# Kernel tuning notes

Measured on AMD Instinct MI355X. Metric: run time of the kernel, lower is better.

## Reference

```python
import jax, jax.numpy as jnp
import numpy as np

SEQ_LEN, BATCH, INPUT_SIZE, HIDDEN_SIZE = 512, 64, 1024, 1024


def setup_inputs() -> dict:
    key = jax.random.key(0)
    k1, k2, k3 = jax.random.split(key, 3)
    inp = jax.random.normal(k1, (SEQ_LEN, BATCH, INPUT_SIZE), dtype=jnp.float32)
    weight_ih = jax.random.normal(k2, (4 * HIDDEN_SIZE, INPUT_SIZE), dtype=jnp.float32) * 0.01
    weight_hh = jax.random.normal(k3, (4 * HIDDEN_SIZE, HIDDEN_SIZE), dtype=jnp.float32) * 0.01
    bias_ih = jnp.zeros((4 * HIDDEN_SIZE,), dtype=jnp.float32)
    bias_hh = jnp.zeros((4 * HIDDEN_SIZE,), dtype=jnp.float32)
    h0 = jnp.zeros((BATCH, HIDDEN_SIZE), dtype=jnp.float32)
    c0 = jnp.zeros((BATCH, HIDDEN_SIZE), dtype=jnp.float32)
    return {"input": inp, "weight_ih": weight_ih, "weight_hh": weight_hh,
            "bias_ih": bias_ih, "bias_hh": bias_hh, "h0": h0, "c0": c0}


def _lstm(input, weight_ih, weight_hh, bias_ih, bias_hh, h0, c0):
    H = weight_hh.shape[1]
    # Precompute input projections for all timesteps in one big GEMM: [T,B,4H]
    x_proj = jnp.einsum('tbi,gi->tbg', input, weight_ih) + bias_ih + bias_hh

    def step(carry, xg_t):
        h_prev, c_prev = carry
        gates = xg_t + h_prev @ weight_hh.T  # [B, 4H]
        i_g = jax.nn.sigmoid(gates[:, 0*H:1*H])
        f_g = jax.nn.sigmoid(gates[:, 1*H:2*H])
        g_g = jnp.tanh(gates[:, 2*H:3*H])
        o_g = jax.nn.sigmoid(gates[:, 3*H:4*H])
        c_cur = f_g * c_prev + i_g * g_g
        h_cur = o_g * jnp.tanh(c_cur)
        return (h_cur, c_cur), h_cur

    (h_last, c_last), outputs = jax.lax.scan(step, (h0, c0), x_proj)
    return outputs, (h_last[None], c_last[None])


def reference(input, weight_ih, weight_hh, bias_ih, bias_hh, h0, c0):
    return _lstm(input, weight_ih, weight_hh, bias_ih, bias_hh, h0, c0)
```

## Files before the change

### kernel.cpp

```cpp
#include <hip/hip_runtime.h>
#include <stdint.h>

#define SEQ    512
#define NBATCH 64
#define HID    1024
#define GDIM   4096

typedef __attribute__((ext_vector_type(4))) float          f32x4;
typedef __attribute__((ext_vector_type(8))) short          s16x8;
typedef __attribute__((ext_vector_type(4))) unsigned short u16x4;
typedef __attribute__((ext_vector_type(4))) unsigned int   u32x4;

#define MFMA_BF16(a,b,c) __builtin_amdgcn_mfma_f32_16x16x32_bf16((a),(b),(c),0,0,0)

__device__ __forceinline__ unsigned short f2bf(float f){
  union { float f; unsigned u; } v; v.f = f;
  unsigned r = v.u + 0x7fffu + ((v.u >> 16) & 1u);
  return (unsigned short)(r >> 16);
}

__device__ __forceinline__ void gload_lds16(const void* g, void* l){
  __builtin_amdgcn_global_load_lds((const __attribute__((address_space(1))) void*)g,
                                   (__attribute__((address_space(3))) void*)l,
                                   16, 0, 0);
}

__global__ __launch_bounds__(256) void cvt_bf16(const float* __restrict__ s,
                                                unsigned short* __restrict__ d, int n4){
  int i = blockIdx.x*256 + threadIdx.x;
  if (i >= n4) return;
  f32x4 v = *(const f32x4*)(s + (size_t)i*4);
  u16x4 o;
  o[0]=f2bf(v[0]); o[1]=f2bf(v[1]); o[2]=f2bf(v[2]); o[3]=f2bf(v[3]);
  *(u16x4*)(d + (size_t)i*4) = o;
}

__global__ __launch_bounds__(256) void init_state(const float* __restrict__ h0,
                                                  const float* __restrict__ c0,
                                                  unsigned short* __restrict__ hring,
                                                  float* __restrict__ cstate){
  int i = blockIdx.x*256 + threadIdx.x;
  hring[i]  = f2bf(h0[i]);
  cstate[i] = c0[i];
}

__global__ __launch_bounds__(256,1) void gemm_xproj(
    const unsigned short* __restrict__ A,
    const unsigned short* __restrict__ Bw,
    const float* __restrict__ bih, const float* __restrict__ bhh,
    float* __restrict__ C, int M)
{
  __shared__ unsigned short Al[2][128*64];
  __shared__ unsigned short Bl[2][128*64];

  const int bm = blockIdx.x >> 5;
  const int bn = blockIdx.x & 31;
  const int tid = threadIdx.x;
  const int wv = tid >> 6, l = tid & 63;
  const int wm = wv >> 1, wn = wv & 1;
  const int c16 = l & 15, rq = l >> 4;

  const unsigned short* Ab = A  + (size_t)bm*128*1024;
  const unsigned short* Bb = Bw + (size_t)bn*128*1024;

  f32x4 acc[4][4];
#pragma unroll
  for (int i=0;i<4;++i)
#pragma unroll
    for (int j=0;j<4;++j) acc[i][j] = (f32x4){0.f,0.f,0.f,0.f};

  auto stage = [&](int buf, int kt){
    const int k0 = kt*64;
    const int rsub = wv*8 + (l>>3);
    const int col  = (l&7)*8;
#pragma unroll
    for (int is=0; is<4; ++is){
      const int row = is*32 + rsub;
      gload_lds16(Ab + (size_t)row*1024 + k0 + col, &Al[buf][row*64 + col]);
      gload_lds16(Bb + (size_t)row*1024 + k0 + col, &Bl[buf][row*64 + col]);
    }
  };

  stage(0, 0);
  asm volatile("s_waitcnt vmcnt(0)" ::: "memory");
  __syncthreads();

  for (int kt = 0; kt < 16; ++kt){
    const int cur = kt & 1;
    if (kt < 15) stage(cur^1, kt+1);
#pragma unroll
    for (int ks=0; ks<2; ++ks){
      s16x8 afr[4], bfr[4];
#pragma unroll
      for (int mi=0;mi<4;++mi)
        afr[mi] = *(const s16x8*)&Al[cur][(wm*64 + mi*16 + c16)*64 + ks*32 + rq*8];
#pragma unroll
      for (int ni=0;ni<4;++ni)
        bfr[ni] = *(const s16x8*)&Bl[cur][(wn*64 + ni*16 + c16)*64 + ks*32 + rq*8];
#pragma unroll
      for (int mi=0;mi<4;++mi)
#pragma unroll
        for (int ni=0;ni<4;++ni)
          acc[mi][ni] = MFMA_BF16(afr[mi], bfr[ni], acc[mi][ni]);
    }
    asm volatile("s_waitcnt vmcnt(0)" ::: "memory");
    __syncthreads();
  }

  const int crow0 = bm*128 + wm*64;
  const int ccol0 = bn*128 + wn*64;
#pragma unroll
  for (int ni=0;ni<4;++ni){
    const int col = ccol0 + ni*16 + c16;
    const float bsum = bih[col] + bhh[col];
#pragma unroll
    for (int mi=0;mi<4;++mi){
      const int row = crow0 + mi*16 + rq*4;
#pragma unroll
      for (int r=0;r<4;++r)
        C[(size_t)(row+r)*GDIM + col] = acc[mi][ni][r] + bsum;
    }
  }
}

__global__ __launch_bounds__(512,1) void lstm_rec(
    const unsigned short* __restrict__ whhb,
    const float* __restrict__ xproj,
    unsigned short* __restrict__ hring,
    float* __restrict__ cstate,
    float* __restrict__ outp,
    unsigned int* __restrict__ bar,
    int t0, int nsteps)
{
  const int tid = threadIdx.x;
  const int wv = tid >> 6, l = tid & 63;
  const int c16 = l & 15, rq = l >> 4;
  const int bq = blockIdx.x >> 6;
  const int hg = blockIdx.x & 63;
  const int hc0 = hg * 16;
  const int b0  = bq * 16;
  const int em = tid >> 4, ec = tid & 15;

  __shared__ float part[2*8*16*68];
  __shared__ __align__(16) unsigned short hsh[256];

  s16x8 breg[4][4];
#pragma unroll
  for (int nt = 0; nt < 4; ++nt){
    const int n = nt*16 + c16;
    const size_t grow = (size_t)(n & 3)*HID + hc0 + (n >> 2);
#pragma unroll
    for (int ks = 0; ks < 4; ++ks)
      breg[nt][ks] = *(const s16x8*)(whhb + grow*HID + wv*128 + ks*32 + rq*8);
  }

  float creg = 0.f, xp[4] = {0.f,0.f,0.f,0.f};
  if (tid < 256){
    creg = cstate[(size_t)(b0+em)*HID + hc0 + ec];
#pragma unroll
    for (int g = 0; g < 4; ++g)
      xp[g] = xproj[(size_t)(b0+em)*GDIM + g*HID + hc0 + ec];
  }

  const unsigned int* fq = bar + ((bq*64 + wv*8 + (l & 7)) << 5);

  for (int t = t0; t < t0 + nsteps; ++t){
    if (l < 8){
      unsigned fv; int spins = 0;
      const unsigned ut = (unsigned)t;
      do {
        asm volatile("global_load_dword %0, %1, off sc0 sc1\n\ts_waitcnt vmcnt(0)"
                     : "=v"(fv) : "v"(fq) : "memory");
        if (fv >= ut) break;
        if (++spins > 2) __builtin_amdgcn_s_sleep(2);
      } while (spins < (1 << 20));
    }

    const unsigned short* hb = hring + (size_t)(t & 1)*65536
                             + (size_t)(b0 + c16)*HID + wv*128 + rq*8;
    u32x4 af[4];
#define AL(K) asm volatile("global_load_dwordx4 %0, %1, off offset:%c2 sc0 sc1" \
                           : "=v"(af[K]) : "v"(hb), "i"((K)*64))
    AL(0); AL(1); AL(2); AL(3);
#undef AL
    asm volatile("s_waitcnt vmcnt(0)" ::: "memory");
    __builtin_amdgcn_sched_barrier(0);

    f32x4 acc[4];
#pragma unroll
    for (int nt = 0; nt < 4; ++nt) acc[nt] = (f32x4){0.f,0.f,0.f,0.f};
#pragma unroll
    for (int ks = 0; ks < 4; ++ks){
      const s16x8 a = __builtin_bit_cast(s16x8, af[ks]);
#pragma unroll
      for (int nt = 0; nt < 4; ++nt)
        acc[nt] = MFMA_BF16(a, breg[nt][ks], acc[nt]);
    }

    const int pbuf = t & 1;
    {
      float* pb = &part[(size_t)(pbuf*8 + wv)*16*68];
#pragma unroll
      for (int nt = 0; nt < 4; ++nt)
#pragma unroll
        for (int r = 0; r < 4; ++r)
          pb[(rq*4 + r)*68 + nt*16 + c16] = acc[nt][r];
    }
    __syncthreads();

    float hval = 0.f;
    if (tid < 256){
      f32x4 vv = (f32x4){xp[0], xp[1], xp[2], xp[3]};
#pragma unroll
      for (int k8 = 0; k8 < 8; ++k8)
        vv += *(const f32x4*)&part[((size_t)(pbuf*8 + k8)*16 + em)*68 + ec*4];
      const float ig = 1.f/(1.f + __expf(-vv[0]));
      const float fg = 1.f/(1.f + __expf(-vv[1]));
      const float gg = tanhf(vv[2]);
      const float og = 1.f/(1.f + __expf(-vv[3]));
      creg = fg*creg + ig*gg;
      hval = og * tanhf(creg);
      hsh[em*16 + ec] = f2bf(hval);
    }
    __syncthreads();

    if (tid < 32){
      const int row = l >> 1, ch = l & 1;
      const unsigned short* hp = hring + (size_t)((t+1) & 1)*65536
                               + (size_t)(b0 + row)*HID + hc0 + ch*8;
      u32x4 hv = *(const u32x4*)&hsh[row*16 + ch*8];
      asm volatile("global_store_dwordx4 %0, %1, off sc0 sc1"
                   :: "v"(hp), "v"(hv) : "memory");
      asm volatile("s_waitcnt vmcnt(0)" ::: "memory");
      if (tid == 0){
        unsigned int* fp = bar + ((unsigned)blockIdx.x << 5);
        unsigned int fv = (unsigned int)(t + 1);
        asm volatile("global_store_dword %0, %1, off sc0 sc1"
                     :: "v"(fp), "v"(fv) : "memory");
      }
    }

    if (tid < 256){
      const size_t oidx = (size_t)(b0+em)*HID + hc0 + ec;
      outp[(size_t)t*65536 + oidx] = hval;
      if (t == SEQ-1){
        outp[(size_t)SEQ*65536 + oidx]         = hval;
        outp[(size_t)SEQ*65536 + 65536 + oidx] = creg;
      }
      if (t+1 < t0 + nsteps){
        const size_t xrow = (size_t)(t+1 - t0)*NBATCH + (b0+em);
#pragma unroll
        for (int g = 0; g < 4; ++g)
          xp[g] = xproj[xrow*GDIM + g*HID + hc0 + ec];
      }
    }
  }

  if (tid < 256)
    cstate[(size_t)(b0+em)*HID + hc0 + ec] = creg;
}

extern "C" void kernel_launch(void* const* d_in, const int* in_sizes, int n_in,
                              void* d_out, int out_size, void* d_ws, size_t ws_size,
                              hipStream_t stream)
{
  const float* inp = (const float*)d_in[0];
  const float* wih = (const float*)d_in[1];
  const float* whh = (const float*)d_in[2];
  const float* bih = (const float*)d_in[3];
  const float* bhh = (const float*)d_in[4];
  const float* h0  = (const float*)d_in[5];
  const float* c0  = (const float*)d_in[6];
  float* outp = (float*)d_out;

  auto alignup = [](size_t x){ return (x + 255) & ~(size_t)255; };
  auto need = [&](size_t ch)->size_t{
    size_t s = 0;
    s += alignup(ch*64*4096*4);
    s += alignup(ch*64*1024*2);
    s += alignup((size_t)4096*1024*2);
    s += alignup((size_t)4096*1024*2);
    s += alignup((size_t)2*64*1024*2);
    s += alignup((size_t)64*1024*4);
    s += alignup((size_t)256*32*4);
    return s;
  };
  int CH = 512;
  while (CH > 2 && need(CH) > ws_size) CH >>= 1;

  char* w = (char*)d_ws;
  float*          xproj  = (float*)w;          w += alignup((size_t)CH*64*4096*4);
  unsigned short* in_bf  = (unsigned short*)w; w += alignup((size_t)CH*64*1024*2);
  unsigned short* wih_bf = (unsigned short*)w; w += alignup((size_t)4096*1024*2);
  unsigned short* whh_bf = (unsigned short*)w; w += alignup((size_t)4096*1024*2);
  unsigned short* hring  = (unsigned short*)w; w += alignup((size_t)2*64*1024*2);
  float*          cst    = (float*)w;          w += alignup((size_t)64*1024*4);
  unsigned int*   bar    = (unsigned int*)w;

  hipMemsetAsync(bar, 0, 256*32*4, stream);

  cvt_bf16<<<4096, 256, 0, stream>>>(wih, wih_bf, 4096*1024/4);
  cvt_bf16<<<4096, 256, 0, stream>>>(whh, whh_bf, 4096*1024/4);
  init_state<<<256, 256, 0, stream>>>(h0, c0, hring, cst);

  const int nch = SEQ / CH;
  for (int ci = 0; ci < nch; ++ci){
    const int t0 = ci * CH;
    const int n4 = CH*64*1024/4;
    cvt_bf16<<<(n4+255)/256, 256, 0, stream>>>(inp + (size_t)t0*65536, in_bf, n4);
    gemm_xproj<<<dim3((CH*64/128)*32), 256, 0, stream>>>(in_bf, wih_bf, bih, bhh,
                                                         xproj, CH*64);
    lstm_rec<<<dim3(256), dim3(512), 0, stream>>>(whh_bf, xproj, hring, cst, outp,
                                                  bar, t0, CH);
  }
}
```

Measured before the change: 2.257 ms.

## Fuse input projection into persistent recurrent kernel with one-step-ahead prefetch

After: 2.322 ms. 2.9% more time.

```diff
diff --git a/kernel.cpp b/kernel.cpp
--- a/kernel.cpp
+++ b/kernel.cpp
@@ -17,12 +17,6 @@
   union { float f; unsigned u; } v; v.f = f;
   unsigned r = v.u + 0x7fffu + ((v.u >> 16) & 1u);
   return (unsigned short)(r >> 16);
-}
-
-__device__ __forceinline__ void gload_lds16(const void* g, void* l){
-  __builtin_amdgcn_global_load_lds((const __attribute__((address_space(1))) void*)g,
-                                   (__attribute__((address_space(3))) void*)l,
-                                   16, 0, 0);
 }
 
 __global__ __launch_bounds__(256) void cvt_bf16(const float* __restrict__ s,
@@ -44,88 +38,11 @@
   cstate[i] = c0[i];
 }
 
-__global__ __launch_bounds__(256,1) void gemm_xproj(
-    const unsigned short* __restrict__ A,
-    const unsigned short* __restrict__ Bw,
-    const float* __restrict__ bih, const float* __restrict__ bhh,
-    float* __restrict__ C, int M)
-{
-  __shared__ unsigned short Al[2][128*64];
-  __shared__ unsigned short Bl[2][128*64];
-
-  const int bm = blockIdx.x >> 5;
-  const int bn = blockIdx.x & 31;
-  const int tid = threadIdx.x;
-  const int wv = tid >> 6, l = tid & 63;
-  const int wm = wv >> 1, wn = wv & 1;
-  const int c16 = l & 15, rq = l >> 4;
-
-  const unsigned short* Ab = A  + (size_t)bm*128*1024;
-  const unsigned short* Bb = Bw + (size_t)bn*128*1024;
-
-  f32x4 acc[4][4];
-#pragma unroll
-  for (int i=0;i<4;++i)
-#pragma unroll
-    for (int j=0;j<4;++j) acc[i][j] = (f32x4){0.f,0.f,0.f,0.f};
-
-  auto stage = [&](int buf, int kt){
-    const int k0 = kt*64;
-    const int rsub = wv*8 + (l>>3);
-    const int col  = (l&7)*8;
-#pragma unroll
-    for (int is=0; is<4; ++is){
-      const int row = is*32 + rsub;
-      gload_lds16(Ab + (size_t)row*1024 + k0 + col, &Al[buf][row*64 + col]);
-      gload_lds16(Bb + (size_t)row*1024 + k0 + col, &Bl[buf][row*64 + col]);
-    }
-  };
-
-  stage(0, 0);
-  asm volatile("s_waitcnt vmcnt(0)" ::: "memory");
-  __syncthreads();
-
-  for (int kt = 0; kt < 16; ++kt){
-    const int cur = kt & 1;
-    if (kt < 15) stage(cur^1, kt+1);
-#pragma unroll
-    for (int ks=0; ks<2; ++ks){
-      s16x8 afr[4], bfr[4];
-#pragma unroll
-      for (int mi=0;mi<4;++mi)
-        afr[mi] = *(const s16x8*)&Al[cur][(wm*64 + mi*16 + c16)*64 + ks*32 + rq*8];
-#pragma unroll
-      for (int ni=0;ni<4;++ni)
-        bfr[ni] = *(const s16x8*)&Bl[cur][(wn*64 + ni*16 + c16)*64 + ks*32 + rq*8];
-#pragma unroll
-      for (int mi=0;mi<4;++mi)
-#pragma unroll
-        for (int ni=0;ni<4;++ni)
-          acc[mi][ni] = MFMA_BF16(afr[mi], bfr[ni], acc[mi][ni]);
-    }
-    asm volatile("s_waitcnt vmcnt(0)" ::: "memory");
-    __syncthreads();
-  }
-
-  const int crow0 = bm*128 + wm*64;
-  const int ccol0 = bn*128 + wn*64;
-#pragma unroll
-  for (int ni=0;ni<4;++ni){
-    const int col = ccol0 + ni*16 + c16;
-    const float bsum = bih[col] + bhh[col];
-#pragma unroll
-    for (int mi=0;mi<4;++mi){
-      const int row = crow0 + mi*16 + rq*4;
-#pragma unroll
-      for (int r=0;r<4;++r)
-        C[(size_t)(row+r)*GDIM + col] = acc[mi][ni][r] + bsum;
-    }
-  }
-}
-
 __global__ __launch_bounds__(512,1) void lstm_rec(
     const unsigned short* __restrict__ whhb,
-    const float* __restrict__ xproj,
+    const unsigned short* __restrict__ wihb,
+    const unsigned short* __restrict__ xbf,
+    const float* __restrict__ bih, const float* __restrict__ bhh,
     unsigned short* __restrict__ hring,
     float* __restrict__ cstate,
     float* __restrict__ outp,
@@ -135,34 +52,64 @@
   const int tid = threadIdx.x;
   const int wv = tid >> 6, l = tid & 63;
   const int c16 = l & 15, rq = l >> 4;
-  const int bq = blockIdx.x >> 6;
-  const int hg = blockIdx.x & 63;
+  const int m8 = blockIdx.x & 7;
+  const int bq = m8 >> 1;
+  const int hg = ((blockIdx.x >> 3) << 1) | (m8 & 1);
   const int hc0 = hg * 16;
   const int b0  = bq * 16;
   const int em = tid >> 4, ec = tid & 15;
 
-  __shared__ float part[2*8*16*68];
+  __shared__ float part_h[2*8*16*68];
+  __shared__ float part_x[2*8*16*68];
   __shared__ __align__(16) unsigned short hsh[256];
 
-  s16x8 breg[4][4];
+  s16x8 bhh_r[4][4], bih_r[4][4];
 #pragma unroll
   for (int nt = 0; nt < 4; ++nt){
     const int n = nt*16 + c16;
     const size_t grow = (size_t)(n & 3)*HID + hc0 + (n >> 2);
 #pragma unroll
-    for (int ks = 0; ks < 4; ++ks)
-      breg[nt][ks] = *(const s16x8*)(whhb + grow*HID + wv*128 + ks*32 + rq*8);
-  }
-
-  float creg = 0.f, xp[4] = {0.f,0.f,0.f,0.f};
+    for (int ks = 0; ks < 4; ++ks){
+      const size_t off = grow*HID + wv*128 + ks*32 + rq*8;
+      bhh_r[nt][ks] = *(const s16x8*)(whhb + off);
+      bih_r[nt][ks] = *(const s16x8*)(wihb + off);
+    }
+  }
+
+  float creg = 0.f, bsum[4] = {0.f,0.f,0.f,0.f};
   if (tid < 256){
     creg = cstate[(size_t)(b0+em)*HID + hc0 + ec];
 #pragma unroll
-    for (int g = 0; g < 4; ++g)
-      xp[g] = xproj[(size_t)(b0+em)*GDIM + g*HID + hc0 + ec];
+    for (int g = 0; g < 4; ++g){
+      const size_t bi = (size_t)g*HID + hc0 + ec;
+      bsum[g] = bih[bi] + bhh[bi];
+    }
   }
 
   const unsigned int* fq = bar + ((bq*64 + wv*8 + (l & 7)) << 5);
+
+  {
+    const unsigned short* xb = xbf + ((size_t)t0*NBATCH + b0 + c16)*HID
+                             + wv*128 + rq*8;
+    s16x8 ax[4];
+#pragma unroll
+    for (int ks = 0; ks < 4; ++ks)
+      ax[ks] = *(const s16x8*)(xb + ks*32);
+    f32x4 accx[4];
+#pragma unroll
+    for (int nt = 0; nt < 4; ++nt) accx[nt] = (f32x4){0.f,0.f,0.f,0.f};
+#pragma unroll
+    for (int ks = 0; ks < 4; ++ks)
+#pragma unroll
+      for (int nt = 0; nt < 4; ++nt)
+        accx[nt] = MFMA_BF16(ax[ks], bih_r[nt][ks], accx[nt]);
+    float* pb = &part_x[(size_t)((t0 & 1)*8 + wv)*16*68];
+#pragma unroll
+    for (int nt = 0; nt < 4; ++nt)
+#pragma unroll
+      for (int r = 0; r < 4; ++r)
+        pb[(rq*4 + r)*68 + nt*16 + c16] = accx[nt][r];
+  }
 
   for (int t = t0; t < t0 + nsteps; ++t){
     if (l < 8){
@@ -183,37 +130,63 @@
                            : "=v"(af[K]) : "v"(hb), "i"((K)*64))
     AL(0); AL(1); AL(2); AL(3);
 #undef AL
+    const int tn = (t+1 < SEQ) ? t+1 : SEQ-1;
+    const unsigned short* xb = xbf + ((size_t)tn*NBATCH + b0 + c16)*HID
+                             + wv*128 + rq*8;
+    u32x4 axr[4];
+#define XL(K) asm volatile("global_load_dwordx4 %0, %1, off offset:%c2" \
+                           : "=v"(axr[K]) : "v"(xb), "i"((K)*64))
+    XL(0); XL(1); XL(2); XL(3);
+#undef XL
+    asm volatile("s_waitcnt vmcnt(4)" ::: "memory");
+    __builtin_amdgcn_sched_barrier(0);
+
+    f32x4 acc[4];
+#pragma unroll
+    for (int nt = 0; nt < 4; ++nt) acc[nt] = (f32x4){0.f,0.f,0.f,0.f};
+#pragma unroll
+    for (int ks = 0; ks < 4; ++ks){
+      const s16x8 a = __builtin_bit_cast(s16x8, af[ks]);
+#pragma unroll
+      for (int nt = 0; nt < 4; ++nt)
+        acc[nt] = MFMA_BF16(a, bhh_r[nt][ks], acc[nt]);
+    }
     asm volatile("s_waitcnt vmcnt(0)" ::: "memory");
     __builtin_amdgcn_sched_barrier(0);
 
-    f32x4 acc[4];
-#pragma unroll
-    for (int nt = 0; nt < 4; ++nt) acc[nt] = (f32x4){0.f,0.f,0.f,0.f};
+    f32x4 accx[4];
+#pragma unroll
+    for (int nt = 0; nt < 4; ++nt) accx[nt] = (f32x4){0.f,0.f,0.f,0.f};
 #pragma unroll
     for (int ks = 0; ks < 4; ++ks){
-      const s16x8 a = __builtin_bit_cast(s16x8, af[ks]);
-#pragma unroll
-      for (int nt = 0; nt < 4; ++nt)
-        acc[nt] = MFMA_BF16(a, breg[nt][ks], acc[nt]);
-    }
-
+      const s16x8 a = __builtin_bit_cast(s16x8, axr[ks]);
+#pragma unroll
+      for (int nt = 0; nt < 4; ++nt)
+        accx[nt] = MFMA_BF16(a, bih_r[nt][ks], accx[nt]);
+    }
+
+    {
+      float* ph = &part_h[(size_t)(((t   ) & 1)*8 + wv)*16*68];
+      float* px = &part_x[(size_t)(((t+1) & 1)*8 + wv)*16*68];
+#pragma unroll
+      for (int nt = 0; nt < 4; ++nt)
+#pragma unroll
+        for (int r = 0; r < 4; ++r){
+          ph[(rq*4 + r)*68 + nt*16 + c16] = acc[nt][r];
+          px[(rq*4 + r)*68 + nt*16 + c16] = accx[nt][r];
+        }
+    }
+    __syncthreads();
+
+    float hval = 0.f;
     const int pbuf = t & 1;
-    {
-      float* pb = &part[(size_t)(pbuf*8 + wv)*16*68];
-#pragma unroll
-      for (int nt = 0; nt < 4; ++nt)
-#pragma unroll
-        for (int r = 0; r < 4; ++r)
-          pb[(rq*4 + r)*68 + nt*16 + c16] = acc[nt][r];
-    }
-    __syncthreads();
-
-    float hval = 0.f;
     if (tid < 256){
-      f32x4 vv = (f32x4){xp[0], xp[1], xp[2], xp[3]};
-#pragma unroll
-      for (int k8 = 0; k8 < 8; ++k8)
-        vv += *(const f32x4*)&part[((size_t)(pbuf*8 + k8)*16 + em)*68 + ec*4];
+      f32x4 vv = (f32x4){bsum[0], bsum[1], bsum[2], bsum[3]};
+#pragma unroll
+      for (int k8 = 0; k8 < 8; ++k8){
+        vv += *(const f32x4*)&part_h[((size_t)(pbuf*8 + k8)*16 + em)*68 + ec*4];
+        vv += *(const f32x4*)&part_x[((size_t)(pbuf*8 + k8)*16 + em)*68 + ec*4];
+      }
       const float ig = 1.f/(1.f + __expf(-vv[0]));
       const float fg = 1.f/(1.f + __expf(-vv[1]));
       const float gg = tanhf(vv[2]);
@@ -233,7 +206,7 @@
                    :: "v"(hp), "v"(hv) : "memory");
       asm volatile("s_waitcnt vmcnt(0)" ::: "memory");
       if (tid == 0){
-        unsigned int* fp = bar + ((unsigned)blockIdx.x << 5);
+        unsigned int* fp = bar + ((bq*64 + hg) << 5);
         unsigned int fv = (unsigned int)(t + 1);
         asm volatile("global_store_dword %0, %1, off sc0 sc1"
                      :: "v"(fp), "v"(fv) : "memory");
@@ -246,12 +219,6 @@
       if (t == SEQ-1){
         outp[(size_t)SEQ*65536 + oidx]         = hval;
         outp[(size_t)SEQ*65536 + 65536 + oidx] = creg;
-      }
-      if (t+1 < t0 + nsteps){
-        const size_t xrow = (size_t)(t+1 - t0)*NBATCH + (b0+em);
-#pragma unroll
-        for (int g = 0; g < 4; ++g)
-          xp[g] = xproj[xrow*GDIM + g*HID + hc0 + ec];
       }
     }
   }
@@ -274,23 +241,8 @@
   float* outp = (float*)d_out;
 
   auto alignup = [](size_t x){ return (x + 255) & ~(size_t)255; };
-  auto need = [&](size_t ch)->size_t{
-    size_t s = 0;
-    s += alignup(ch*64*4096*4);
-    s += alignup(ch*64*1024*2);
-    s += alignup((size_t)4096*1024*2);
-    s += alignup((size_t)4096*1024*2);
-    s += alignup((size_t)2*64*1024*2);
-    s += alignup((size_t)64*1024*4);
-    s += alignup((size_t)256*32*4);
-    return s;
-  };
-  int CH = 512;
-  while (CH > 2 && need(CH) > ws_size) CH >>= 1;
-
   char* w = (char*)d_ws;
-  float*          xproj  = (float*)w;          w += alignup((size_t)CH*64*4096*4);
-  unsigned short* in_bf  = (unsigned short*)w; w += alignup((size_t)CH*64*1024*2);
+  unsigned short* in_bf  = (unsigned short*)w; w += alignup((size_t)SEQ*64*1024*2);
   unsigned short* wih_bf = (unsigned short*)w; w += alignup((size_t)4096*1024*2);
   unsigned short* whh_bf = (unsigned short*)w; w += alignup((size_t)4096*1024*2);
   unsigned short* hring  = (unsigned short*)w; w += alignup((size_t)2*64*1024*2);
@@ -299,18 +251,11 @@
 
   hipMemsetAsync(bar, 0, 256*32*4, stream);
 
+  cvt_bf16<<<SEQ*64*1024/4/256, 256, 0, stream>>>(inp, in_bf, SEQ*64*1024/4);
   cvt_bf16<<<4096, 256, 0, stream>>>(wih, wih_bf, 4096*1024/4);
   cvt_bf16<<<4096, 256, 0, stream>>>(whh, whh_bf, 4096*1024/4);
   init_state<<<256, 256, 0, stream>>>(h0, c0, hring, cst);
 
-  const int nch = SEQ / CH;
-  for (int ci = 0; ci < nch; ++ci){
-    const int t0 = ci * CH;
-    const int n4 = CH*64*1024/4;
-    cvt_bf16<<<(n4+255)/256, 256, 0, stream>>>(inp + (size_t)t0*65536, in_bf, n4);
-    gemm_xproj<<<dim3((CH*64/128)*32), 256, 0, stream>>>(in_bf, wih_bf, bih, bhh,
-                                                         xproj, CH*64);
-    lstm_rec<<<dim3(256), dim3(512), 0, stream>>>(whh_bf, xproj, hring, cst, outp,
-                                                  bar, t0, CH);
-  }
-}
+  lstm_rec<<<dim3(256), dim3(512), 0, stream>>>(whh_bf, wih_bf, in_bf, bih, bhh,
+                                                hring, cst, outp, bar, 0, SEQ);
+}
```
